# Optimization experiments

Measured on AMD Instinct MI355X. Metric: run time of the kernel, lower is better.

The kernel has to match this reference:

```python
import jax, jax.numpy as jnp
import numpy as np

NA = 5            # num_anchors
NC = 13           # num_classes
COORD_SCALE = 1.0
NOOBJ_SCALE = 1.0
OBJ_SCALE = 5.0
# corner_confidence9 constants (singleshotpose defaults)
TH = 80.0
SHARP = 2.0
IMW = 640.0
IMH = 480.0


def _forward(output, target):
    nB, _, nH, nW = output.shape
    out = output.reshape(nB, NA, 19 + NC, nH, nW)
    # channels 0,1 sigmoided in-place in the torch code; 2..17 raw
    xys_pred = jnp.concatenate([jax.nn.sigmoid(out[:, :, 0:2]), out[:, :, 2:18]], axis=2)  # [nB,nA,18,nH,nW]
    conf = jax.nn.sigmoid(out[:, :, 18])  # [nB,nA,nH,nW]

    # --- build_targets (done on output.data / target.data in torch -> stop_gradient) ---
    pc = jax.lax.stop_gradient(xys_pred)
    gxr = jnp.arange(nW, dtype=pc.dtype)
    gyr = jnp.arange(nH, dtype=pc.dtype)
    px = (pc[:, :, 0::2] + gxr[None, None, None, None, :]) / nW  # [nB,nA,9,nH,nW] normalized x corners
    py = (pc[:, :, 1::2] + gyr[None, None, None, :, None]) / nH  # [nB,nA,9,nH,nW] normalized y corners

    tgt = jax.lax.stop_gradient(target).reshape(nB, 50, 21)
    coords = tgt[:, :, 1:19]  # [nB,50,18] normalized gt corners (x0,y0,...,x8,y8)
    # torch loop breaks at first zero x0 -> prefix-valid mask
    valid = jnp.cumprod((coords[:, :, 0] != 0).astype(jnp.int32), axis=1).astype(bool)
    gi = jnp.floor(coords[:, :, 0] * nW).astype(jnp.int32)  # [nB,50]
    gj = jnp.floor(coords[:, :, 1] * nH).astype(jnp.int32)

    b_idx = jnp.broadcast_to(jnp.arange(nB)[:, None], (nB, 50))
    # predicted box at assigned cell, anchor best_n = 0 (as in source)
    prx = px[b_idx, 0, :, gj, gi]  # [nB,50,9]
    pry = py[b_idx, 0, :, gj, gi]
    pbox = jnp.stack([prx, pry], axis=-1).reshape(nB, 50, 18)

    # corner_confidence9 (singleshotpose): mean of thresholded exp-distance conf over 9 corners
    d = (coords - pbox).reshape(nB, 50, 9, 2) * jnp.array([IMW, IMH], dtype=coords.dtype)
    dn = jnp.sqrt(jnp.sum(d * d, axis=-1))  # [nB,50,9] pixel distances
    cvals = (jnp.exp(SHARP * (1.0 - dn / TH)) - 1.0) * (dn < TH).astype(coords.dtype)
    conf_t = jnp.mean(cvals, axis=-1) / (jnp.exp(jnp.asarray(SHARP, coords.dtype)) - 1.0 + 1e-5)  # [nB,50]

    # route invalid targets out of bounds -> dropped by scatter
    gi_s = jnp.where(valid, gi, nW)
    gj_s = jnp.where(valid, gj, nH)
    bf = b_idx.reshape(-1)
    gif = gi_s.reshape(-1)
    gjf = gj_s.reshape(-1)

    coord_mask = jnp.zeros((nB, NA, nH, nW), output.dtype).at[bf, 0, gjf, gif].set(1.0)
    conf_mask = jnp.full((nB, NA, nH, nW), NOOBJ_SCALE, output.dtype).at[bf, 0, gjf, gif].set(OBJ_SCALE)
    tconf = jnp.zeros((nB, NA, nH, nW), output.dtype).at[bf, 0, gjf, gif].set(conf_t.reshape(-1))

    tx = coords[:, :, 0::2] * nW - gi[..., None].astype(coords.dtype)  # [nB,50,9]
    ty = coords[:, :, 1::2] * nH - gj[..., None].astype(coords.dtype)
    tvals = jnp.stack([tx, ty], axis=-1).reshape(nB * 50, 18)
    tar = jnp.zeros((nB, NA, 18, nH, nW), output.dtype).at[bf, 0, :, gjf, gif].set(tvals)

    # --- losses ---
    cm = coord_mask[:, :, None]  # [nB,nA,1,nH,nW]
    loss_xy = COORD_SCALE * jnp.sum((xys_pred * cm - tar * cm) ** 2) / 2.0
    cms = jnp.sqrt(conf_mask)
    loss_conf = jnp.sum((conf * cms - tconf * cms) ** 2) / 2.0
    return loss_xy + loss_conf


def setup_inputs() -> dict:
    key = jax.random.key(0)
    k1, k2 = jax.random.split(key)
    output = jax.random.normal(k1, (32, NA * (19 + NC), 76, 76), dtype=jnp.float32)
    target = jax.random.uniform(k2, (32, 50 * 21), dtype=jnp.float32)
    return {"output": output, "target": target}


def reference(output, target):
    return _forward(output, target)
```

## Files before the change

kernel.cpp:

```cpp
#include <hip/hip_runtime.h>
#include <math.h>

#define NB 32
#define NA 5
#define NC 13
#define NHH 76
#define NWW 76
#define NT 50
#define CH (19 + NC)
#define CELLS (NHH * NWW)
#define NBA (NB * NA)
#define V4_PER_SLAB (CELLS / 4)
#define SWEEP_BLOCKS NBA
#define GRID_BLOCKS (SWEEP_BLOCKS + NB)

#define OBJ_SCALE 5.0f
#define TH_ 80.0f
#define SHARP_ 2.0f
#define IMW_ 640.0f
#define IMH_ 480.0f

#define POISON64 0xAAAAAAAAAAAAAAAAull

__device__ __forceinline__ float sigmoidf_(float x) {
    return 1.0f / (1.0f + expf(-x));
}

__global__ void main_kernel(const float* __restrict__ outp,
                            const float* __restrict__ tgt,
                            unsigned long long* __restrict__ ws64,
                            float* __restrict__ out) {
    int bid = blockIdx.x;
    int tid = threadIdx.x;
    double local = 0.0;

    if (bid < SWEEP_BLOCKS) {
        const float4* slab =
            (const float4*)(outp + ((size_t)bid * CH + 18) * CELLS);
        for (int r = tid; r < V4_PER_SLAB; r += 256) {
            float4 q = slab[r];
            float a0 = sigmoidf_(q.x), a1 = sigmoidf_(q.y);
            float a2 = sigmoidf_(q.z), a3 = sigmoidf_(q.w);
            local += 0.5 * (double)(a0 * a0 + a1 * a1 + a2 * a2 + a3 * a3);
        }
    } else {
        int b = bid - SWEEP_BLOCKS;
        __shared__ int sgi[NT], sgj[NT], snz[NT], svalid[NT];

        if (tid < NT) {
            const float* tg = tgt + (size_t)(b * NT + tid) * 21;
            float cx = tg[1];
            float cy = tg[2];
            sgi[tid] = (int)floorf(cx * (float)NWW);
            sgj[tid] = (int)floorf(cy * (float)NHH);
            snz[tid] = (cx != 0.0f) ? 1 : 0;
        }
        __syncthreads();
        if (tid < NT) {
            int v = 1;
            for (int k = 0; k <= tid; ++k) v &= snz[k];
            svalid[tid] = v;
        }
        __syncthreads();

        if (tid < NT) {
            int gi = sgi[tid], gj = sgj[tid];
            bool inb = (gi >= 0 && gi < NWW && gj >= 0 && gj < NHH);
            bool win = svalid[tid] && inb;
            if (win) {
                for (int k2 = tid + 1; k2 < NT; ++k2) {
                    if (svalid[k2] && sgi[k2] == gi && sgj[k2] == gj) { win = false; break; }
                }
            }
            if (win) {
                const float* tg = tgt + (size_t)(b * NT + tid) * 21;
                int cell = gj * NWW + gi;
                const float* base = outp + (size_t)b * NA * CH * CELLS;

                float v[19];
                #pragma unroll
                for (int c = 0; c < 19; ++c) v[c] = base[(size_t)c * CELLS + cell];
                float s0 = sigmoidf_(v[0]);
                float s1 = sigmoidf_(v[1]);
                float confv = sigmoidf_(v[18]);

                const float denom = expf(SHARP_) - 1.0f + 1e-5f;
                float ssum = 0.0f;
                #pragma unroll
                for (int k = 0; k < 9; ++k) {
                    float vx = (k == 0) ? s0 : v[2 * k];
                    float vy = (k == 0) ? s1 : v[2 * k + 1];
                    float px = (vx + (float)gi) / (float)NWW;
                    float py = (vy + (float)gj) / (float)NHH;
                    float dx = (tg[1 + 2 * k] - px) * IMW_;
                    float dy = (tg[2 + 2 * k] - py) * IMH_;
                    float dn = sqrtf(dx * dx + dy * dy);
                    if (dn < TH_) ssum += expf(SHARP_ * (1.0f - dn / TH_)) - 1.0f;
                }
                float conf_t = (ssum / 9.0f) / denom;

                float cs = 0.0f;
                #pragma unroll
                for (int k = 0; k < 9; ++k) {
                    float tvx = tg[1 + 2 * k] * (float)NWW - (float)gi;
                    float tvy = tg[2 + 2 * k] * (float)NHH - (float)gj;
                    float dx = ((k == 0) ? s0 : v[2 * k]) - tvx;
                    float dy = ((k == 0) ? s1 : v[2 * k + 1]) - tvy;
                    cs += dx * dx + dy * dy;
                }

                float dc = confv - conf_t;
                local = 0.5 * (double)(OBJ_SCALE * dc * dc - confv * confv + cs);
            }
        }
    }

    __shared__ double sdata[256];
    sdata[tid] = local;
    __syncthreads();
    for (int s = 128; s > 0; s >>= 1) {
        if (tid < s) sdata[tid] += sdata[tid + s];
        __syncthreads();
    }

    if (tid == 0) {
        double* acc = (double*)&ws64[0];
        unsigned long long* cnt = &ws64[1];

        double old_acc = atomicAdd(acc, sdata[0]);
        asm volatile("" : : "v"(old_acc));
        asm volatile("s_waitcnt vmcnt(0)" ::: "memory");

        unsigned long long oc = atomicAdd(cnt, 1ull);

        if (oc == (unsigned long long)(GRID_BLOCKS - 1) ||
            oc == POISON64 + (unsigned long long)(GRID_BLOCKS - 1)) {
            unsigned long long bits = atomicExch(&ws64[0], POISON64);
            double total = __longlong_as_double(bits);
            out[0] = (float)total;
            atomicExch(cnt, POISON64);
        }
    }
}

extern "C" void kernel_launch(void* const* d_in, const int* in_sizes, int n_in,
                              void* d_out, int out_size, void* d_ws, size_t ws_size,
                              hipStream_t stream) {
    const float* outp = (const float*)d_in[0];
    const float* tgt  = (const float*)d_in[1];
    float* out = (float*)d_out;
    unsigned long long* ws64 = (unsigned long long*)d_ws;

    main_kernel<<<GRID_BLOCKS, 256, 0, stream>>>(outp, tgt, ws64, out);
}
```

Measured before the change: 18.82 us.

## Split confidence sweep across more blocks, use wave shuffles and striped atomic slots

Each per-anchor confidence slab is now split across 6 blocks, and each thread handles a single float4 instead of looping. This fills more compute units than the previous 160 sweep blocks. The shared-memory tree reduction becomes a wavefront shuffle reduction plus a 4-entry shared sum. The global accumulation is spread over 8 padded double slots to reduce atomic contention. The trade-off is many more blocks hitting the shared completion counter, and a final pass that reads and clears all 8 slots.

New measurement: 22.25 us. 18.2% more time.

```diff
diff --git a/kernel.cpp b/kernel.cpp
--- a/kernel.cpp
+++ b/kernel.cpp
@@ -11,7 +11,8 @@
 #define CELLS (NHH * NWW)
 #define NBA (NB * NA)
 #define V4_PER_SLAB (CELLS / 4)
-#define SWEEP_BLOCKS NBA
+#define BLK_PER_SLAB 6
+#define SWEEP_BLOCKS (NBA * BLK_PER_SLAB)
 #define GRID_BLOCKS (SWEEP_BLOCKS + NB)
 
 #define OBJ_SCALE 5.0f
@@ -21,6 +22,9 @@
 #define IMH_ 480.0f
 
 #define POISON64 0xAAAAAAAAAAAAAAAAull
+#define NSLOT 8
+#define SLOT_STRIDE 16
+#define CNT_IDX (NSLOT * SLOT_STRIDE)
 
 __device__ __forceinline__ float sigmoidf_(float x) {
     return 1.0f / (1.0f + expf(-x));
@@ -35,13 +39,16 @@
     double local = 0.0;
 
     if (bid < SWEEP_BLOCKS) {
-        const float4* slab =
-            (const float4*)(outp + ((size_t)bid * CH + 18) * CELLS);
-        for (int r = tid; r < V4_PER_SLAB; r += 256) {
-            float4 q = slab[r];
+        int slab = bid / BLK_PER_SLAB;
+        int part = bid - slab * BLK_PER_SLAB;
+        int idx = part * 256 + tid;
+        if (idx < V4_PER_SLAB) {
+            const float4* sl =
+                (const float4*)(outp + ((size_t)slab * CH + 18) * CELLS);
+            float4 q = sl[idx];
             float a0 = sigmoidf_(q.x), a1 = sigmoidf_(q.y);
             float a2 = sigmoidf_(q.z), a3 = sigmoidf_(q.w);
-            local += 0.5 * (double)(a0 * a0 + a1 * a1 + a2 * a2 + a3 * a3);
+            local = 0.5 * (double)(a0 * a0 + a1 * a1 + a2 * a2 + a3 * a3);
         }
     } else {
         int b = bid - SWEEP_BLOCKS;
@@ -115,19 +122,21 @@
         }
     }
 
-    __shared__ double sdata[256];
-    sdata[tid] = local;
+    #pragma unroll
+    for (int off = 32; off > 0; off >>= 1)
+        local += __shfl_down(local, off, 64);
+
+    __shared__ double swave[4];
+    int wave = tid >> 6;
+    if ((tid & 63) == 0) swave[wave] = local;
     __syncthreads();
-    for (int s = 128; s > 0; s >>= 1) {
-        if (tid < s) sdata[tid] += sdata[tid + s];
-        __syncthreads();
-    }
 
     if (tid == 0) {
-        double* acc = (double*)&ws64[0];
-        unsigned long long* cnt = &ws64[1];
+        double partial = swave[0] + swave[1] + swave[2] + swave[3];
+        double* acc = (double*)&ws64[(bid & (NSLOT - 1)) * SLOT_STRIDE];
+        unsigned long long* cnt = &ws64[CNT_IDX];
 
-        double old_acc = atomicAdd(acc, sdata[0]);
+        double old_acc = atomicAdd(acc, partial);
         asm volatile("" : : "v"(old_acc));
         asm volatile("s_waitcnt vmcnt(0)" ::: "memory");
 
@@ -135,8 +144,13 @@
 
         if (oc == (unsigned long long)(GRID_BLOCKS - 1) ||
             oc == POISON64 + (unsigned long long)(GRID_BLOCKS - 1)) {
-            unsigned long long bits = atomicExch(&ws64[0], POISON64);
-            double total = __longlong_as_double(bits);
+            double total = 0.0;
+            #pragma unroll
+            for (int i = 0; i < NSLOT; ++i) {
+                unsigned long long bits =
+                    atomicExch(&ws64[i * SLOT_STRIDE], POISON64);
+                total += __longlong_as_double(bits);
+            }
             out[0] = (float)total;
             atomicExch(cnt, POISON64);
         }
```
